# Optimization experiments

Measured on AMD Instinct MI355X. Metric: run time of the kernel, lower is better.

The kernel has to match this reference:

```python
import jax, jax.numpy as jnp
import numpy as np

NODES = 16384                       # power of two -> all heap levels complete
DEPTH = (NODES - 1).bit_length() + 1  # 15 heap steps, linears k = 0..14
IN_F = 64
OUT_F = 64
MINHEAP = 0
BATCH = 32


def setup_inputs() -> dict:
    key = jax.random.key(0)
    k1, k2, k3 = jax.random.split(key, 3)
    x = jax.random.normal(k1, (BATCH, NODES, IN_F), dtype=jnp.float32)
    # stacked per-heap-step Linear params, torch layout W: [out, in]
    W = jax.random.normal(k2, (DEPTH - MINHEAP, OUT_F, IN_F), dtype=jnp.float32) * 0.05
    b = jax.random.normal(k3, (DEPTH - MINHEAP, OUT_F), dtype=jnp.float32) * 0.05
    return {"x": x, "W": W, "b": b}


def reference(x, W, b):
    # HeapLinear forward. Heap layout: level l occupies nodes [2^(l-1), 2^l)
    # (root = node 0, level(j) = bit_length(j)). The original double loop over
    # (input level l, linear k) with repeat_interleave(2^k) is equivalent to:
    #   output[j] = sum_{k=minheap}^{depth-1, level(j)>=k} linears[k](input[j >> k])
    # for power-of-two `nodes` (every out block satisfies out_node1 <= nodes).
    nodes = x.shape[-2]
    depth = (nodes - 1).bit_length() + 1
    j = np.arange(nodes)
    levels = np.array([int(v).bit_length() for v in j])  # static, trace-time
    out = jnp.zeros(x.shape[:-1] + (W.shape[1],), dtype=x.dtype)
    for k in range(MINHEAP, depth):
        n_anc = max(nodes >> k, 1)  # only nodes 0..n_anc-1 serve as distance-k ancestors
        # small per-level Linear applied to ancestor slice: [..., n_anc, out]
        t = jnp.einsum('...ni,oi->...no', x[..., :n_anc, :], W[k - MINHEAP]) + b[k - MINHEAP]
        anc = j >> k                      # distance-k ancestor of each node
        mask = levels >= k                # nodes shallower than k have no such ancestor
        out = out + jnp.where(mask[:, None], t[..., anc, :], jnp.zeros((), x.dtype))
    return out
```

## Files before the change

kernel.cpp:

```cpp
#include <hip/hip_runtime.h>

#define NODES 16384
#define NF 64
#define NBLK 128
#define TROW 72
#define BATCH 32

#define WS_WBF_OFF    0ull
#define WS_BPRE_OFF   122880ull
#define WS_NEEDED     126720ull

typedef __attribute__((ext_vector_type(8))) short short8;
typedef __attribute__((ext_vector_type(4))) short shortx4;
typedef __attribute__((ext_vector_type(4))) float floatx4;

__device__ __forceinline__ short f2bf(float f) {
    unsigned u = __float_as_uint(f);
    u += 0x7fffu + ((u >> 16) & 1u);
    return (short)(u >> 16);
}
__device__ __forceinline__ float bf2f(short s) {
    return __uint_as_float(((unsigned)(unsigned short)s) << 16);
}
__device__ __forceinline__ short8 cvt8(floatx4 a, floatx4 c) {
    short8 r;
    r[0]=f2bf(a[0]); r[1]=f2bf(a[1]); r[2]=f2bf(a[2]); r[3]=f2bf(a[3]);
    r[4]=f2bf(c[0]); r[5]=f2bf(c[1]); r[6]=f2bf(c[2]); r[7]=f2bf(c[3]);
    return r;
}

__global__ __launch_bounds__(256)
void heaplin_prep(const float* __restrict__ W, const float* __restrict__ bias,
                  short* __restrict__ wbf, float* __restrict__ bpre)
{
    const int blk = blockIdx.x;
    const int tid = threadIdx.x;
    if (blk < 30) {
        int e = blk * 2048 + tid * 8;
        floatx4 a = *(const floatx4*)(W + e);
        floatx4 c = *(const floatx4*)(W + e + 4);
        *(short8*)(wbf + e) = cvt8(a, c);
    } else if (tid < 64) {
        float run = 0.f;
        for (int k = 0; k < 15; ++k) { run += bias[k * 64 + tid]; bpre[k * 64 + tid] = run; }
    }
}

__global__ __launch_bounds__(256, 2)
void heaplin_main(const float* __restrict__ x, const float* __restrict__ W,
                  const short* __restrict__ wbf,
                  const float* __restrict__ bpre, float* __restrict__ out)
{
    __shared__ short tbuf[128 * TROW];
    __shared__ float farpart[4 * 64];

    const int tid  = threadIdx.x;
    const int lane = tid & 63;
    const int wave = tid >> 6;
    const int lr = lane & 15;
    const int lq = lane >> 4;
    const int nblk = blockIdx.x;
    const int b    = blockIdx.y;
    const float* xb = x + (size_t)b * NODES * NF;
    float* ob = out + (size_t)b * NODES * NF;
    const floatx4 zero4 = {0.f, 0.f, 0.f, 0.f};

    if (nblk == 0) {
        floatx4 accE[8];
        #pragma unroll
        for (int t8 = 0; t8 < 8; ++t8) accE[t8] = zero4;

        for (int k = 0; k < 8; ++k) {
            __syncthreads();
            #pragma unroll
            for (int i = 0; i < 8; ++i) {
                int job = tid + i * 256;
                int r = job >> 4, c4 = job & 15;
                bool valid = (k == 0) || (r >= (1 << (k - 1)));
                floatx4 vv = zero4;
                if (valid) vv = *(const floatx4*)(xb + (r >> k) * NF + c4 * 4);
                shortx4 s4;
                s4[0]=f2bf(vv[0]); s4[1]=f2bf(vv[1]); s4[2]=f2bf(vv[2]); s4[3]=f2bf(vv[3]);
                *(shortx4*)(tbuf + r * TROW + c4 * 4) = s4;
            }
            __syncthreads();
            #pragma unroll
            for (int t8 = 0; t8 < 8; ++t8) {
                int mt = 2 * wave + (t8 & 1);
                int nt = t8 >> 1;
                int arow = mt * 16 + lr;
                const short* wp = wbf + k * 4096 + (nt * 16 + lr) * 64 + lq * 8;
                short8 b0 = *(const short8*)wp;
                short8 b1 = *(const short8*)(wp + 32);
                short8 a0 = *(const short8*)(tbuf + arow * TROW + lq * 8);
                short8 a1 = *(const short8*)(tbuf + arow * TROW + 32 + lq * 8);
                accE[t8] = __builtin_amdgcn_mfma_f32_16x16x32_bf16(a0, b0, accE[t8], 0, 0, 0);
                accE[t8] = __builtin_amdgcn_mfma_f32_16x16x32_bf16(a1, b1, accE[t8], 0, 0, 0);
            }
        }
        #pragma unroll
        for (int t8 = 0; t8 < 8; ++t8) {
            int mt = 2 * wave + (t8 & 1);
            int nt = t8 >> 1;
            int c = nt * 16 + lr;
            #pragma unroll
            for (int rg = 0; rg < 4; ++rg) {
                int j = mt * 16 + lq * 4 + rg;
                int lvl = (j == 0) ? 0 : (32 - __clz(j));
                ob[(size_t)j * NF + c] = accE[t8][rg] + bpre[lvl * 64 + c];
            }
        }
        return;
    }

    const int n0 = nblk * NBLK;
    const int L  = 32 - __clz(n0);

    floatx4 accE[8];
    {
        const float* apA = xb + (size_t)(n0 + 2 * wave * 16 + lr) * NF + lq * 8;
        const float* apB = apA + 16 * NF;
        floatx4 fA0 = *(const floatx4*)apA,        fA1 = *(const floatx4*)(apA + 4);
        floatx4 fA2 = *(const floatx4*)(apA + 32), fA3 = *(const floatx4*)(apA + 36);
        floatx4 fB0 = *(const floatx4*)apB,        fB1 = *(const floatx4*)(apB + 4);
        floatx4 fB2 = *(const floatx4*)(apB + 32), fB3 = *(const floatx4*)(apB + 36);
        short8 aA0 = cvt8(fA0, fA1), aA1 = cvt8(fA2, fA3);
        short8 aB0 = cvt8(fB0, fB1), aB1 = cvt8(fB2, fB3);
        #pragma unroll
        for (int nt = 0; nt < 4; ++nt) {
            const short* wp = wbf + (nt * 16 + lr) * 64 + lq * 8;
            short8 b0 = *(const short8*)wp;
            short8 b1 = *(const short8*)(wp + 32);
            floatx4 accA = zero4, accB = zero4;
            accA = __builtin_amdgcn_mfma_f32_16x16x32_bf16(aA0, b0, accA, 0, 0, 0);
            accA = __builtin_amdgcn_mfma_f32_16x16x32_bf16(aA1, b1, accA, 0, 0, 0);
            accB = __builtin_amdgcn_mfma_f32_16x16x32_bf16(aB0, b0, accB, 0, 0, 0);
            accB = __builtin_amdgcn_mfma_f32_16x16x32_bf16(aB1, b1, accB, 0, 0, 0);
            accE[2 * nt + 0] = accA;
            accE[2 * nt + 1] = accB;
        }
    }

    {
        float p = 0.f;
        const int q = wave, o = lane;
        #pragma unroll
        for (int k = 8; k <= 14; ++k) {
            const float* xa = xb + (size_t)(n0 >> k) * NF + q * 16;
            const float* wr = W + k * 4096 + o * 64 + q * 16;
            float s = 0.f;
            #pragma unroll
            for (int i = 0; i < 4; ++i) {
                floatx4 wv = *(const floatx4*)(wr + i * 4);
                floatx4 xv = *(const floatx4*)(xa + i * 4);
                s += wv[0]*xv[0] + wv[1]*xv[1] + wv[2]*xv[2] + wv[3]*xv[3];
            }
            p += (k <= L) ? s : 0.f;
        }
        if (q == 0) p += bpre[L * 64 + o];
        farpart[q * 64 + o] = p;
    }

    #pragma unroll
    for (int g = 0; g < 3; ++g) {
        const int idx = wave + g * 4;
        const bool gvalid = (idx < 11);
        const int idxc = gvalid ? idx : 0;
        int k, mt;
        if (idxc < 4)       { k = 1; mt = idxc; }
        else if (idxc < 6)  { k = 2; mt = idxc - 4; }
        else if (idxc == 6) { k = 3; mt = 0; }
        else                { k = idxc - 3; mt = 0; }
        const int anc = n0 >> k;
        const int rowb = (anc & ~15) + mt * 16;
        const float* ap = xb + (size_t)(rowb + lr) * NF + lq * 8;
        floatx4 f0 = *(const floatx4*)ap,        f1 = *(const floatx4*)(ap + 4);
        floatx4 f2 = *(const floatx4*)(ap + 32), f3 = *(const floatx4*)(ap + 36);
        short8 a0 = cvt8(f0, f1), a1 = cvt8(f2, f3);
        const int tb  = 128 - (256 >> k);
        const int cnt = 128 >> k;
        const int off = anc & 15;
        #pragma unroll
        for (int nt = 0; nt < 4; ++nt) {
            const short* wp = wbf + k * 4096 + (nt * 16 + lr) * 64 + lq * 8;
            short8 b0 = *(const short8*)wp;
            short8 b1 = *(const short8*)(wp + 32);
            floatx4 acc = zero4;
            acc = __builtin_amdgcn_mfma_f32_16x16x32_bf16(a0, b0, acc, 0, 0, 0);
            acc = __builtin_amdgcn_mfma_f32_16x16x32_bf16(a1, b1, acc, 0, 0, 0);
            if (gvalid) {
                #pragma unroll
                for (int rg = 0; rg < 4; ++rg) {
                    int m = lq * 4 + rg;
                    if (k <= 3) {
                        tbuf[(tb + mt * 16 + m) * TROW + nt * 16 + lr] = f2bf(acc[rg]);
                    } else if (m >= off && m < off + cnt) {
                        tbuf[(tb + m - off) * TROW + nt * 16 + lr] = f2bf(acc[rg]);
                    }
                }
            }
        }
    }
    __syncthreads();

    {
        int m  = tid >> 2;
        int c0 = (tid & 3) * 16;
        float e[16];
        #pragma unroll
        for (int i = 0; i < 16; ++i) {
            int c = c0 + i;
            e[i] = bf2f(tbuf[ m               * TROW + c])
                 + bf2f(tbuf[(64  + (m >> 1)) * TROW + c])
                 + bf2f(tbuf[(96  + (m >> 2)) * TROW + c])
                 + bf2f(tbuf[(112 + (m >> 3)) * TROW + c])
                 + bf2f(tbuf[(120 + (m >> 4)) * TROW + c])
                 + bf2f(tbuf[(124 + (m >> 5)) * TROW + c])
                 + bf2f(tbuf[126              * TROW + c])
                 + farpart[c] + farpart[64 + c] + farpart[128 + c] + farpart[192 + c];
        }
        #pragma unroll
        for (int i = 0; i < 16; ++i) tbuf[m * TROW + c0 + i] = f2bf(e[i]);
    }
    __syncthreads();

    #pragma unroll
    for (int t8 = 0; t8 < 8; ++t8) {
        int mt = 2 * wave + (t8 & 1);
        int nt = t8 >> 1;
        int c = nt * 16 + lr;
        #pragma unroll
        for (int rg = 0; rg < 4; ++rg) {
            int j = mt * 16 + lq * 4 + rg;
            float val = accE[t8][rg] + bf2f(tbuf[(j >> 1) * TROW + c]);
            ob[(size_t)(n0 + j) * NF + c] = val;
        }
    }
}

#define SROW 72
#define SROWS 270
__global__ __launch_bounds__(256, 4)
void heaplin_fallback(const float* __restrict__ x, const float* __restrict__ W,
                      const float* __restrict__ bias, float* __restrict__ out)
{
    __shared__ short stage[SROWS * SROW];
    __shared__ float farpart[4 * 64];
    short* tbuf = stage;
    float* cumB = (float*)(stage + 128 * SROW);

    const int tid  = threadIdx.x;
    const int lane = tid & 63;
    const int wave = tid >> 6;
    const int lr = lane & 15;
    const int lq = lane >> 4;
    const int nblk = blockIdx.x;
    const int b    = blockIdx.y;
    const float* xb = x + (size_t)b * NODES * NF;
    float* ob = out + (size_t)b * NODES * NF;
    const floatx4 zero4 = {0.f, 0.f, 0.f, 0.f};

    if (nblk == 0) {
        if (tid < 64) {
            float run = 0.f;
            for (int k = 0; k < 15; ++k) { run += bias[k * 64 + tid]; cumB[k * 64 + tid] = run; }
        }
        floatx4 accE[8];
        #pragma unroll
        for (int t8 = 0; t8 < 8; ++t8) accE[t8] = zero4;
        for (int k = 0; k < 8; ++k) {
            __syncthreads();
            #pragma unroll
            for (int i = 0; i < 8; ++i) {
                int job = tid + i * 256;
                int r = job >> 4, c4 = job & 15;
                bool valid = (k == 0) || (r >= (1 << (k - 1)));
                floatx4 vv = zero4;
                if (valid) vv = *(const floatx4*)(xb + (r >> k) * NF + c4 * 4);
                shortx4 s4;
                s4[0]=f2bf(vv[0]); s4[1]=f2bf(vv[1]); s4[2]=f2bf(vv[2]); s4[3]=f2bf(vv[3]);
                *(shortx4*)(stage + r * SROW + c4 * 4) = s4;
            }
            __syncthreads();
            #pragma unroll
            for (int t8 = 0; t8 < 8; ++t8) {
                int mt = 2 * wave + (t8 & 1);
                int nt = t8 >> 1;
                int arow = mt * 16 + lr;
                const float* wr = W + k * 4096 + (nt * 16 + lr) * 64 + lq * 8;
                floatx4 wa = *(const floatx4*)wr, wb2 = *(const floatx4*)(wr + 4);
                short8 b0 = cvt8(wa, wb2);
                floatx4 wc = *(const floatx4*)(wr + 32), wd = *(const floatx4*)(wr + 36);
                short8 b1 = cvt8(wc, wd);
                short8 a0 = *(const short8*)(stage + arow * SROW + lq * 8);
                short8 a1 = *(const short8*)(stage + arow * SROW + 32 + lq * 8);
                accE[t8] = __builtin_amdgcn_mfma_f32_16x16x32_bf16(a0, b0, accE[t8], 0, 0, 0);
                accE[t8] = __builtin_amdgcn_mfma_f32_16x16x32_bf16(a1, b1, accE[t8], 0, 0, 0);
            }
        }
        #pragma unroll
        for (int t8 = 0; t8 < 8; ++t8) {
            int mt = 2 * wave + (t8 & 1);
            int nt = t8 >> 1;
            int c = nt * 16 + lr;
            #pragma unroll
            for (int rg = 0; rg < 4; ++rg) {
                int j = mt * 16 + lq * 4 + rg;
                int lvl = (j == 0) ? 0 : (32 - __clz(j));
                ob[(size_t)j * NF + c] = accE[t8][rg] + cumB[lvl * 64 + c];
            }
        }
        return;
    }

    const int n0 = nblk * NBLK;
    const int L  = 32 - __clz(n0);
    floatx4 v[16];
    #pragma unroll
    for (int i = 0; i < 16; ++i) {
        int job = tid + i * 256;
        int r = job >> 4, c4 = job & 15;
        int node;
        if (r < 128)        node = n0 + r;
        else if (r >= 254)  node = n0 >> 7;
        else { int k = __clz(255 - r) - 24; node = (n0 >> k) + r - (256 - (256 >> k)); }
        v[i] = *(const floatx4*)(xb + (size_t)node * NF + c4 * 4);
    }
    #pragma unroll
    for (int i = 0; i < 16; ++i) {
        int job = tid + i * 256;
        int r = job >> 4, c4 = job & 15;
        shortx4 s4;
        s4[0]=f2bf(v[i][0]); s4[1]=f2bf(v[i][1]); s4[2]=f2bf(v[i][2]); s4[3]=f2bf(v[i][3]);
        *(shortx4*)(stage + r * SROW + c4 * 4) = s4;
    }
    __syncthreads();
    floatx4 accE[8];
    #pragma unroll
    for (int t8 = 0; t8 < 8; ++t8) {
        int mt = 2 * wave + (t8 & 1);
        int nt = t8 >> 1;
        int arow = mt * 16 + lr;
        const float* wr = W + (nt * 16 + lr) * 64 + lq * 8;
        floatx4 wa = *(const floatx4*)wr, wb2 = *(const floatx4*)(wr + 4);
        short8 b0 = cvt8(wa, wb2);
        floatx4 wc = *(const floatx4*)(wr + 32), wd = *(const floatx4*)(wr + 36);
        short8 b1 = cvt8(wc, wd);
        short8 a0 = *(const short8*)(stage + arow * SROW + lq * 8);
        short8 a1 = *(const short8*)(stage + arow * SROW + 32 + lq * 8);
        floatx4 acc = zero4;
        acc = __builtin_amdgcn_mfma_f32_16x16x32_bf16(a0, b0, acc, 0, 0, 0);
        acc = __builtin_amdgcn_mfma_f32_16x16x32_bf16(a1, b1, acc, 0, 0, 0);
        accE[t8] = acc;
    }
    {
        float p = 0.f;
        const int q = wave, o = lane;
        for (int k = 8; k <= L; ++k) {
            const float* xa = xb + (size_t)(n0 >> k) * NF + q * 16;
            const float* wr = W + k * 4096 + o * 64 + q * 16;
            #pragma unroll
            for (int i = 0; i < 4; ++i) {
                floatx4 wv = *(const floatx4*)(wr + i * 4);
                floatx4 xv = *(const floatx4*)(xa + i * 4);
                p += wv[0]*xv[0] + wv[1]*xv[1] + wv[2]*xv[2] + wv[3]*xv[3];
            }
        }
        if (q == 0) for (int k = 0; k <= L; ++k) p += bias[k * 64 + o];
        farpart[q * 64 + o] = p;
    }
    __syncthreads();
    for (int jj = 0; jj < 11; ++jj) {
        int job = wave + jj * 4;
        int idx = job % 11;
        int nt  = job / 11;
        int k, mt;
        if (idx < 4)      { k = 1; mt = idx; }
        else if (idx < 6) { k = 2; mt = idx - 4; }
        else if (idx < 7) { k = 3; mt = 0; }
        else              { k = idx - 3; mt = 0; }
        int sbase = 256 - (256 >> k);
        int arow = sbase + mt * 16 + lr;
        const float* wr = W + k * 4096 + (nt * 16 + lr) * 64 + lq * 8;
        floatx4 wa = *(const floatx4*)wr, wb2 = *(const floatx4*)(wr + 4);
        short8 b0 = cvt8(wa, wb2);
        floatx4 wc = *(const floatx4*)(wr + 32), wd = *(const floatx4*)(wr + 36);
        short8 b1 = cvt8(wc, wd);
        short8 a0 = *(const short8*)(stage + arow * SROW + lq * 8);
        short8 a1 = *(const short8*)(stage + arow * SROW + 32 + lq * 8);
        floatx4 acc = zero4;
        acc = __builtin_amdgcn_mfma_f32_16x16x32_bf16(a0, b0, acc, 0, 0, 0);
        acc = __builtin_amdgcn_mfma_f32_16x16x32_bf16(a1, b1, acc, 0, 0, 0);
        int tb = 128 - (256 >> k);
        int nvalid = 128 >> k;
        #pragma unroll
        for (int rg = 0; rg < 4; ++rg) {
            int m = mt * 16 + lq * 4 + rg;
            if (m < nvalid) tbuf[(tb + m) * TROW + nt * 16 + lr] = f2bf(acc[rg]);
        }
    }
    __syncthreads();
    {
        int m  = tid >> 2;
        int c0 = (tid & 3) * 16;
        float e[16];
        #pragma unroll
        for (int i = 0; i < 16; ++i) {
            int c = c0 + i;
            e[i] = bf2f(tbuf[ m               * TROW + c])
                 + bf2f(tbuf[(64  + (m >> 1)) * TROW + c])
                 + bf2f(tbuf[(96  + (m >> 2)) * TROW + c])
                 + bf2f(tbuf[(112 + (m >> 3)) * TROW + c])
                 + bf2f(tbuf[(120 + (m >> 4)) * TROW + c])
                 + bf2f(tbuf[(124 + (m >> 5)) * TROW + c])
                 + bf2f(tbuf[126              * TROW + c])
                 + farpart[c] + farpart[64 + c] + farpart[128 + c] + farpart[192 + c];
        }
        #pragma unroll
        for (int i = 0; i < 16; ++i) tbuf[m * TROW + c0 + i] = f2bf(e[i]);
    }
    __syncthreads();
    #pragma unroll
    for (int t8 = 0; t8 < 8; ++t8) {
        int mt = 2 * wave + (t8 & 1);
        int nt = t8 >> 1;
        int c = nt * 16 + lr;
        #pragma unroll
        for (int rg = 0; rg < 4; ++rg) {
            int j = mt * 16 + lq * 4 + rg;
            float val = accE[t8][rg] + bf2f(tbuf[(j >> 1) * TROW + c]);
            ob[(size_t)(n0 + j) * NF + c] = val;
        }
    }
}

extern "C" void kernel_launch(void* const* d_in, const int* in_sizes, int n_in,
                              void* d_out, int out_size, void* d_ws, size_t ws_size,
                              hipStream_t stream) {
    const float* x  = (const float*)d_in[0];
    const float* W  = (const float*)d_in[1];
    const float* bs = (const float*)d_in[2];
    float* out = (float*)d_out;
    dim3 grid(NODES / NBLK, BATCH);
    if (ws_size >= WS_NEEDED) {
        short* wbf  = (short*)((char*)d_ws + WS_WBF_OFF);
        float* bpre = (float*)((char*)d_ws + WS_BPRE_OFF);
        heaplin_prep<<<31, 256, 0, stream>>>(W, bs, wbf, bpre);
        heaplin_main<<<grid, 256, 0, stream>>>(x, W, wbf, bpre, out);
    } else {
        heaplin_fallback<<<grid, 256, 0, stream>>>(x, W, bs, out);
    }
}
```

Before: 353.5 us.

## Precompute far-ancestor contributions per batch in a separate prep kernel

Adds a second prep kernel that computes, once per batch, the contributions of ancestor levels k>=8 (plus the bias prefix) for each of the 128 node blocks. A transposed fp32 weight copy is staged in workspace for this. The main kernel no longer does the per-block fp32 dot products over W for those far levels. It loads one precomputed vector instead and moves the self MFMA after the ancestor stage. This removes redundant far-level work repeated across all 128 blocks, at the cost of an extra launch, more workspace, and a serial dependency before the main kernel.

```diff
diff --git a/kernel.cpp b/kernel.cpp
--- a/kernel.cpp
+++ b/kernel.cpp
@@ -6,9 +6,11 @@
 #define TROW 72
 #define BATCH 32
 
-#define WS_WBF_OFF    0ull
-#define WS_BPRE_OFF   122880ull
-#define WS_NEEDED     126720ull
+#define WS_WBF_OFF   0ull
+#define WS_WT_OFF    122880ull
+#define WS_BPRE_OFF  368640ull
+#define WS_FAR_OFF   372480ull
+#define WS_NEEDED    1421056ull
 
 typedef __attribute__((ext_vector_type(8))) short short8;
 typedef __attribute__((ext_vector_type(4))) short shortx4;
@@ -30,8 +32,9 @@
 }
 
 __global__ __launch_bounds__(256)
-void heaplin_prep(const float* __restrict__ W, const float* __restrict__ bias,
-                  short* __restrict__ wbf, float* __restrict__ bpre)
+void heaplin_prep1(const float* __restrict__ W, const float* __restrict__ bias,
+                   short* __restrict__ wbf, float* __restrict__ wt,
+                   float* __restrict__ bpre)
 {
     const int blk = blockIdx.x;
     const int tid = threadIdx.x;
@@ -40,19 +43,88 @@
         floatx4 a = *(const floatx4*)(W + e);
         floatx4 c = *(const floatx4*)(W + e + 4);
         *(short8*)(wbf + e) = cvt8(a, c);
-    } else if (tid < 64) {
-        float run = 0.f;
-        for (int k = 0; k < 15; ++k) { run += bias[k * 64 + tid]; bpre[k * 64 + tid] = run; }
+    } else if (blk == 30) {
+        if (tid < 64) {
+            float run = 0.f;
+            for (int k = 0; k < 15; ++k) { run += bias[k * 64 + tid]; bpre[k * 64 + tid] = run; }
+        }
+    } else {
+        int k = blk - 31;
+        #pragma unroll
+        for (int it = 0; it < 16; ++it) {
+            int idx = tid + it * 256;
+            int o = idx >> 6, i = idx & 63;
+            wt[k * 4096 + i * 64 + o] = W[k * 4096 + idx];
+        }
+    }
+}
+
+__global__ __launch_bounds__(256)
+void heaplin_prep2(const float* __restrict__ x, const float* __restrict__ wt,
+                   const float* __restrict__ bpre, float* __restrict__ far)
+{
+    __shared__ float xl[64 * 64];
+    __shared__ float Zl[127 * 64];
+    const int tid = threadIdx.x;
+    const int b   = blockIdx.x;
+    const float* xb = x + (size_t)b * NODES * NF;
+
+    #pragma unroll
+    for (int i = 0; i < 4; ++i) {
+        int job = tid + i * 256;
+        *(floatx4*)(xl + job * 4) = *(const floatx4*)(xb + job * 4);
+    }
+    __syncthreads();
+
+    const int wave = tid >> 6, lane = tid & 63;
+    const int o4 = lane & 15, j = lane >> 4;
+    for (int r = wave; r < 127; r += 4) {
+        int t, a;
+        if (r < 64)       { t = 1; a = r; }
+        else if (r < 96)  { t = 2; a = r - 64; }
+        else if (r < 112) { t = 3; a = r - 96; }
+        else if (r < 120) { t = 4; a = r - 112; }
+        else if (r < 124) { t = 5; a = r - 120; }
+        else if (r < 126) { t = 6; a = r - 124; }
+        else              { t = 7; a = 0; }
+        const float* wtk = wt + (7 + t) * 4096;
+        floatx4 acc = {0.f, 0.f, 0.f, 0.f};
+        #pragma unroll
+        for (int i16 = 0; i16 < 16; ++i16) {
+            int i = j + i16 * 4;
+            floatx4 w4 = *(const floatx4*)(wtk + i * 64 + o4 * 4);
+            float xs = xl[a * 64 + i];
+            acc[0] += w4[0]*xs; acc[1] += w4[1]*xs; acc[2] += w4[2]*xs; acc[3] += w4[3]*xs;
+        }
+        #pragma unroll
+        for (int c = 0; c < 4; ++c) {
+            acc[c] += __shfl_xor(acc[c], 16, 64);
+            acc[c] += __shfl_xor(acc[c], 32, 64);
+        }
+        if (j == 0) *(floatx4*)(Zl + r * 64 + o4 * 4) = acc;
+    }
+    __syncthreads();
+
+    for (int it = 0; it < 32; ++it) {
+        int job = tid + it * 256;
+        if (job < 127 * 64) {
+            int m = 1 + (job >> 6), o = job & 63;
+            int bl = 32 - __clz(m);
+            float s = bpre[(7 + bl) * 64 + o];
+            #pragma unroll
+            for (int t = 1; t <= 7; ++t)
+                if (t <= bl) s += Zl[(128 - (128 >> (t - 1)) + (m >> t)) * 64 + o];
+            far[((size_t)b * 128 + m) * 64 + o] = s;
+        }
     }
 }
 
 __global__ __launch_bounds__(256, 2)
-void heaplin_main(const float* __restrict__ x, const float* __restrict__ W,
-                  const short* __restrict__ wbf,
-                  const float* __restrict__ bpre, float* __restrict__ out)
+void heaplin_main(const float* __restrict__ x, const short* __restrict__ wbf,
+                  const float* __restrict__ far, const float* __restrict__ bpre,
+                  float* __restrict__ out)
 {
     __shared__ short tbuf[128 * TROW];
-    __shared__ float farpart[4 * 64];
 
     const int tid  = threadIdx.x;
     const int lane = tid & 63;
@@ -114,52 +186,6 @@
     }
 
     const int n0 = nblk * NBLK;
-    const int L  = 32 - __clz(n0);
-
-    floatx4 accE[8];
-    {
-        const float* apA = xb + (size_t)(n0 + 2 * wave * 16 + lr) * NF + lq * 8;
-        const float* apB = apA + 16 * NF;
-        floatx4 fA0 = *(const floatx4*)apA,        fA1 = *(const floatx4*)(apA + 4);
-        floatx4 fA2 = *(const floatx4*)(apA + 32), fA3 = *(const floatx4*)(apA + 36);
-        floatx4 fB0 = *(const floatx4*)apB,        fB1 = *(const floatx4*)(apB + 4);
-        floatx4 fB2 = *(const floatx4*)(apB + 32), fB3 = *(const floatx4*)(apB + 36);
-        short8 aA0 = cvt8(fA0, fA1), aA1 = cvt8(fA2, fA3);
-        short8 aB0 = cvt8(fB0, fB1), aB1 = cvt8(fB2, fB3);
-        #pragma unroll
-        for (int nt = 0; nt < 4; ++nt) {
-            const short* wp = wbf + (nt * 16 + lr) * 64 + lq * 8;
-            short8 b0 = *(const short8*)wp;
-            short8 b1 = *(const short8*)(wp + 32);
-            floatx4 accA = zero4, accB = zero4;
-            accA = __builtin_amdgcn_mfma_f32_16x16x32_bf16(aA0, b0, accA, 0, 0, 0);
-            accA = __builtin_amdgcn_mfma_f32_16x16x32_bf16(aA1, b1, accA, 0, 0, 0);
-            accB = __builtin_amdgcn_mfma_f32_16x16x32_bf16(aB0, b0, accB, 0, 0, 0);
-            accB = __builtin_amdgcn_mfma_f32_16x16x32_bf16(aB1, b1, accB, 0, 0, 0);
-            accE[2 * nt + 0] = accA;
-            accE[2 * nt + 1] = accB;
-        }
-    }
-
-    {
-        float p = 0.f;
-        const int q = wave, o = lane;
-        #pragma unroll
-        for (int k = 8; k <= 14; ++k) {
-            const float* xa = xb + (size_t)(n0 >> k) * NF + q * 16;
-            const float* wr = W + k * 4096 + o * 64 + q * 16;
-            float s = 0.f;
-            #pragma unroll
-            for (int i = 0; i < 4; ++i) {
-                floatx4 wv = *(const floatx4*)(wr + i * 4);
-                floatx4 xv = *(const floatx4*)(xa + i * 4);
-                s += wv[0]*xv[0] + wv[1]*xv[1] + wv[2]*xv[2] + wv[3]*xv[3];
-            }
-            p += (k <= L) ? s : 0.f;
-        }
-        if (q == 0) p += bpre[L * 64 + o];
-        farpart[q * 64 + o] = p;
-    }
 
     #pragma unroll
     for (int g = 0; g < 3; ++g) {
@@ -201,26 +227,59 @@
             }
         }
     }
-    __syncthreads();
-
+
+    floatx4 accE[8];
     {
-        int m  = tid >> 2;
-        int c0 = (tid & 3) * 16;
+        const float* apA = xb + (size_t)(n0 + 2 * wave * 16 + lr) * NF + lq * 8;
+        const float* apB = apA + 16 * NF;
+        floatx4 fA0 = *(const floatx4*)apA,        fA1 = *(const floatx4*)(apA + 4);
+        floatx4 fA2 = *(const floatx4*)(apA + 32), fA3 = *(const floatx4*)(apA + 36);
+        floatx4 fB0 = *(const floatx4*)apB,        fB1 = *(const floatx4*)(apB + 4);
+        floatx4 fB2 = *(const floatx4*)(apB + 32), fB3 = *(const floatx4*)(apB + 36);
+        short8 aA0 = cvt8(fA0, fA1), aA1 = cvt8(fA2, fA3);
+        short8 aB0 = cvt8(fB0, fB1), aB1 = cvt8(fB2, fB3);
+        #pragma unroll
+        for (int nt = 0; nt < 4; ++nt) {
+            const short* wp = wbf + (nt * 16 + lr) * 64 + lq * 8;
+            short8 b0 = *(const short8*)wp;
+            short8 b1 = *(const short8*)(wp + 32);
+            floatx4 accA = zero4, accB = zero4;
+            accA = __builtin_amdgcn_mfma_f32_16x16x32_bf16(aA0, b0, accA, 0, 0, 0);
+            accA = __builtin_amdgcn_mfma_f32_16x16x32_bf16(aA1, b1, accA, 0, 0, 0);
+            accB = __builtin_amdgcn_mfma_f32_16x16x32_bf16(aB0, b0, accB, 0, 0, 0);
+            accB = __builtin_amdgcn_mfma_f32_16x16x32_bf16(aB1, b1, accB, 0, 0, 0);
+            accE[2 * nt + 0] = accA;
+            accE[2 * nt + 1] = accB;
+        }
+    }
+
+    const int mD  = tid >> 2;
+    const int c0D = (tid & 3) * 16;
+    floatx4 fvv[4];
+    {
+        const float* fv = far + ((size_t)b * 128 + nblk) * 64 + c0D;
+        #pragma unroll
+        for (int i = 0; i < 4; ++i) fvv[i] = *(const floatx4*)(fv + i * 4);
+    }
+    __syncthreads();
+
+    {
         float e[16];
         #pragma unroll
         for (int i = 0; i < 16; ++i) {
-            int c = c0 + i;
-            e[i] = bf2f(tbuf[ m               * TROW + c])
-                 + bf2f(tbuf[(64  + (m >> 1)) * TROW + c])
-                 + bf2f(tbuf[(96  + (m >> 2)) * TROW + c])
-                 + bf2f(tbuf[(112 + (m >> 3)) * TROW + c])
-                 + bf2f(tbuf[(120 + (m >> 4)) * TROW + c])
-                 + bf2f(tbuf[(124 + (m >> 5)) * TROW + c])
-                 + bf2f(tbuf[126              * TROW + c])
-                 + farpart[c] + farpart[64 + c] + farpart[128 + c] + farpart[192 + c];
-        }
-        #pragma unroll
-        for (int i = 0; i < 16; ++i) tbuf[m * TROW + c0 + i] = f2bf(e[i]);
+            int c = c0D + i;
+            e[i] = bf2f(tbuf[ mD               * TROW + c])
+                 + bf2f(tbuf[(64  + (mD >> 1)) * TROW + c])
+                 + bf2f(tbuf[(96  + (mD >> 2)) * TROW + c])
+                 + bf2f(tbuf[(112 + (mD >> 3)) * TROW + c])
+                 + bf2f(tbuf[(120 + (mD >> 4)) * TROW + c])
+                 + bf2f(tbuf[(124 + (mD >> 5)) * TROW + c])
+                 + bf2f(tbuf[126               * TROW + c])
+                 + fvv[i >> 2][i & 3];
+        }
+        __syncthreads();
+        #pragma unroll
+        for (int i = 0; i < 16; ++i) tbuf[mD * TROW + c0D + i] = f2bf(e[i]);
     }
     __syncthreads();
 
@@ -444,9 +503,12 @@
     dim3 grid(NODES / NBLK, BATCH);
     if (ws_size >= WS_NEEDED) {
         short* wbf  = (short*)((char*)d_ws + WS_WBF_OFF);
+        float* wt   = (float*)((char*)d_ws + WS_WT_OFF);
         float* bpre = (float*)((char*)d_ws + WS_BPRE_OFF);
-        heaplin_prep<<<31, 256, 0, stream>>>(W, bs, wbf, bpre);
-        heaplin_main<<<grid, 256, 0, stream>>>(x, W, wbf, bpre, out);
+        float* farb = (float*)((char*)d_ws + WS_FAR_OFF);
+        heaplin_prep1<<<46, 256, 0, stream>>>(W, bs, wbf, wt, bpre);
+        heaplin_prep2<<<32, 256, 0, stream>>>(x, wt, bpre, farb);
+        heaplin_main<<<grid, 256, 0, stream>>>(x, wbf, farb, bpre, out);
     } else {
         heaplin_fallback<<<grid, 256, 0, stream>>>(x, W, bs, out);
     }
```

New measurement: 332.3 us. -6.0%, faster.
